# Kernel optimization log

Hardware: AMD Instinct MI355X
Metric: run time of the kernel (lower is better)

The kernel has to match this reference:

```python
import jax, jax.numpy as jnp
import numpy as np

BLOCK = 8  # block_size from init_kwargs


def _zigzag(n):
    # Same traversal as zigzag_indices() in the original module.
    idx = np.zeros(n * n, dtype=np.int64)
    i = j = 0
    for k in range(n * n):
        idx[k] = i * n + j
        if (i + j) % 2 == 0:  # moving up-right
            if j == n - 1:
                i += 1
            elif i == 0:
                j += 1
            else:
                i -= 1
                j += 1
        else:  # moving down-left
            if i == n - 1:
                j += 1
            elif j == 0:
                i += 1
            else:
                i += 1
                j -= 1
    return idx


def _dct_basis(N):
    # dct() with norm=None is DCT-II: V[k] = 2 * sum_n x[n] cos(pi*(2n+1)k/(2N))
    k = np.arange(N)[:, None].astype(np.float64)
    nn = np.arange(N)[None, :].astype(np.float64)
    return (2.0 * np.cos(np.pi * (2.0 * nn + 1.0) * k / (2.0 * N))).astype(np.float32)


def setup_inputs() -> dict:
    key = jax.random.key(0)
    img = jax.random.normal(key, (16, 3, 512, 512), dtype=jnp.float32)
    return {"img": img}


def reference(img):
    B = BLOCK
    bs, c, h, w = img.shape
    hb, wb = h // B, w // B
    n = hb * wb
    m = hb  # square grid: m = sqrt(n)

    # split_blocks: unfold(2,B,B).unfold(3,B,B) -> [bs,c,hb,wb,B,B] -> [bs,n,c,B,B]
    blocks = (
        img.reshape(bs, c, hb, B, wb, B)
        .transpose(0, 2, 4, 1, 3, 5)
        .reshape(bs, n, c, B, B)
    )

    # dct_2d with norm=None as separable matmuls against the DCT-II basis
    C = jnp.asarray(_dct_basis(B))  # [B, B] basis, C[k, x]
    z = jnp.einsum("uh,vw,bnchw->bncuv", C, C, blocks)  # [bs,n,c,B,B]

    # frequencyFeat: zigzag-reorder the B*B coeffs, then tile blocks into an m x m map
    zz = jnp.asarray(_zigzag(B))
    flat = z.reshape(bs, n, c, B * B)[..., zz]  # [bs,n,c,B*B]
    feat = (
        flat.reshape(bs, m, m, c, B * B)
        .transpose(0, 3, 4, 1, 2)
        .reshape(bs, c * B * B, m, m)
    )
    return feat
```

## Files before the change

### kernel.cpp

```cpp
#include <hip/hip_runtime.h>


#define K1 1.9615705608064609f
#define K2 1.8477590650225735f
#define K3 1.6629392246050905f
#define K4 1.4142135623730951f
#define K5 1.1111404660392044f
#define K6 0.7653668647301796f
#define K7 0.3901806440322565f

#define DCT8(x0,x1,x2,x3,x4,x5,x6,x7, y0,y1,y2,y3,y4,y5,y6,y7) do {        \
    float s0=(x0)+(x7), s1=(x1)+(x6), s2=(x2)+(x5), s3=(x3)+(x4);          \
    float d0=(x0)-(x7), d1=(x1)-(x6), d2=(x2)-(x5), d3=(x3)-(x4);          \
    float e0=s0+s3, e1=s1+s2, o0=s0-s3, o1=s1-s2;                          \
    y0 = 2.0f*(e0+e1);                                                     \
    y4 = K4*(e0-e1);                                                       \
    y2 = K2*o0 + K6*o1;                                                    \
    y6 = K6*o0 - K2*o1;                                                    \
    y1 = K1*d0 + K3*d1 + K5*d2 + K7*d3;                                    \
    y3 = K3*d0 - K7*d1 - K1*d2 - K5*d3;                                    \
    y5 = K5*d0 - K1*d1 + K7*d2 + K3*d3;                                    \
    y7 = K7*d0 - K5*d1 + K3*d2 - K1*d3;                                    \
} while (0)

#define LOADROW(r)                                                          \
    const float4 L##r##a = *reinterpret_cast<const float4*>(src + (r)*512); \
    const float4 L##r##b = *reinterpret_cast<const float4*>(src + (r)*512 + 4);

#define ROWDCT(r)                                                          \
    DCT8(L##r##a.x,L##r##a.y,L##r##a.z,L##r##a.w,                          \
         L##r##b.x,L##r##b.y,L##r##b.z,L##r##b.w,                          \
         t##r##0,t##r##1,t##r##2,t##r##3,t##r##4,t##r##5,t##r##6,t##r##7);

#define COLSTORE(v, p0,p1,p2,p3,p4,p5,p6,p7) do {                          \
    float z0,z1,z2,z3,z4,z5,z6,z7;                                         \
    DCT8(t0##v,t1##v,t2##v,t3##v,t4##v,t5##v,t6##v,t7##v,                  \
         z0,z1,z2,z3,z4,z5,z6,z7);                                         \
    __builtin_nontemporal_store(z0, dst + (size_t)(p0)*4096);              \
    __builtin_nontemporal_store(z1, dst + (size_t)(p1)*4096);              \
    __builtin_nontemporal_store(z2, dst + (size_t)(p2)*4096);              \
    __builtin_nontemporal_store(z3, dst + (size_t)(p3)*4096);              \
    __builtin_nontemporal_store(z4, dst + (size_t)(p4)*4096);              \
    __builtin_nontemporal_store(z5, dst + (size_t)(p5)*4096);              \
    __builtin_nontemporal_store(z6, dst + (size_t)(p6)*4096);              \
    __builtin_nontemporal_store(z7, dst + (size_t)(p7)*4096);              \
} while (0)

__global__ __launch_bounds__(256) void dct2d_zigzag_kernel(
    const float* __restrict__ img, float* __restrict__ out)
{
    const int tid = blockIdx.x * 256 + threadIdx.x;
    const int bj = tid & 63;
    const int bi = (tid >> 6) & 63;
    const int bc = tid >> 12;

    const float* __restrict__ src =
        img + (size_t)bc * 262144 + (size_t)bi * 4096 + (size_t)bj * 8;

    float* __restrict__ dst =
        out + (size_t)bc * 262144 + (size_t)bi * 64 + (size_t)bj;

    LOADROW(0) LOADROW(1) LOADROW(2) LOADROW(3)
    LOADROW(4) LOADROW(5) LOADROW(6) LOADROW(7)

    float t00,t01,t02,t03,t04,t05,t06,t07;
    float t10,t11,t12,t13,t14,t15,t16,t17;
    float t20,t21,t22,t23,t24,t25,t26,t27;
    float t30,t31,t32,t33,t34,t35,t36,t37;
    float t40,t41,t42,t43,t44,t45,t46,t47;
    float t50,t51,t52,t53,t54,t55,t56,t57;
    float t60,t61,t62,t63,t64,t65,t66,t67;
    float t70,t71,t72,t73,t74,t75,t76,t77;

    ROWDCT(0) ROWDCT(1) ROWDCT(2) ROWDCT(3)
    ROWDCT(4) ROWDCT(5) ROWDCT(6) ROWDCT(7)

    COLSTORE(0,  0,  2,  3,  9, 10, 20, 21, 35);
    COLSTORE(1,  1,  4,  8, 11, 19, 22, 34, 36);
    COLSTORE(2,  5,  7, 12, 18, 23, 33, 37, 48);
    COLSTORE(3,  6, 13, 17, 24, 32, 38, 47, 49);
    COLSTORE(4, 14, 16, 25, 31, 39, 46, 50, 57);
    COLSTORE(5, 15, 26, 30, 40, 45, 51, 56, 58);
    COLSTORE(6, 27, 29, 41, 44, 52, 55, 59, 62);
    COLSTORE(7, 28, 42, 43, 53, 54, 60, 61, 63);
}

extern "C" void kernel_launch(void* const* d_in, const int* in_sizes, int n_in,
                              void* d_out, int out_size, void* d_ws, size_t ws_size,
                              hipStream_t stream)
{
    const float* img = (const float*)d_in[0];
    float* out = (float*)d_out;
    dct2d_zigzag_kernel<<<768, 256, 0, stream>>>(img, out);
}
```

Measured before the change: 95.39 us.

## Stage zigzag outputs through LDS to emit 16-byte nontemporal vector stores

Each thread still computes one 8x8 block DCT, but the coefficients now go to shared memory in groups of 16 zigzag planes. Each wave then reads back contiguous 256-float rows and writes them to global memory as float4 nontemporal stores. Previously each coefficient was a scalar 4-byte store. Wider stores reduce the number of store instructions and memory transactions. The cost is 16KB of LDS per block and eight barriers, which may reduce occupancy and add synchronisation stalls.

Measured after the change: 96.24 us. Within noise of the previous version (+0.9%).

```diff
diff --git a/kernel.cpp b/kernel.cpp
--- a/kernel.cpp
+++ b/kernel.cpp
@@ -1,5 +1,7 @@
 #include <hip/hip_runtime.h>
 
+
+typedef float floatx4 __attribute__((ext_vector_type(4)));
 
 #define K1 1.9615705608064609f
 #define K2 1.8477590650225735f
@@ -32,33 +34,44 @@
          L##r##b.x,L##r##b.y,L##r##b.z,L##r##b.w,                          \
          t##r##0,t##r##1,t##r##2,t##r##3,t##r##4,t##r##5,t##r##6,t##r##7);
 
-#define COLSTORE(v, p0,p1,p2,p3,p4,p5,p6,p7) do {                          \
-    float z0,z1,z2,z3,z4,z5,z6,z7;                                         \
+#define COLDCT(v)                                                          \
     DCT8(t0##v,t1##v,t2##v,t3##v,t4##v,t5##v,t6##v,t7##v,                  \
-         z0,z1,z2,z3,z4,z5,z6,z7);                                         \
-    __builtin_nontemporal_store(z0, dst + (size_t)(p0)*4096);              \
-    __builtin_nontemporal_store(z1, dst + (size_t)(p1)*4096);              \
-    __builtin_nontemporal_store(z2, dst + (size_t)(p2)*4096);              \
-    __builtin_nontemporal_store(z3, dst + (size_t)(p3)*4096);              \
-    __builtin_nontemporal_store(z4, dst + (size_t)(p4)*4096);              \
-    __builtin_nontemporal_store(z5, dst + (size_t)(p5)*4096);              \
-    __builtin_nontemporal_store(z6, dst + (size_t)(p6)*4096);              \
-    __builtin_nontemporal_store(z7, dst + (size_t)(p7)*4096);              \
+         t0##v,t1##v,t2##v,t3##v,t4##v,t5##v,t6##v,t7##v);
+
+#define LW(u,v,p) lds[((p)&15)*256 + tx] = t##u##v;
+
+#define DRAIN(c) do {                                                      \
+    __syncthreads();                                                       \
+    _Pragma("unroll")                                                      \
+    for (int i = 0; i < 4; ++i) {                                          \
+        const int pl = (tx >> 6) * 4 + i;                \
+        const floatx4 vv =                                                 \
+            *reinterpret_cast<const floatx4*>(&lds[pl*256 + lane*4]);      \
+        __builtin_nontemporal_store(vv,                                    \
+            reinterpret_cast<floatx4*>(dstc + (size_t)((c)*16+pl)*4096     \
+                                       + lane*4));                         \
+    }                                                                      \
+    __syncthreads();                                                       \
 } while (0)
 
 __global__ __launch_bounds__(256) void dct2d_zigzag_kernel(
     const float* __restrict__ img, float* __restrict__ out)
 {
-    const int tid = blockIdx.x * 256 + threadIdx.x;
-    const int bj = tid & 63;
-    const int bi = (tid >> 6) & 63;
-    const int bc = tid >> 12;
+    __shared__ float lds[16 * 256];
+
+    const int tx   = threadIdx.x;
+    const int lane = tx & 63;
+    const int w    = tx >> 6;
+    const int g    = blockIdx.x;
+    const int bc   = g >> 4;
+    const int bi0  = (g & 15) * 4;
+    const int bi   = bi0 + w;
 
     const float* __restrict__ src =
-        img + (size_t)bc * 262144 + (size_t)bi * 4096 + (size_t)bj * 8;
+        img + (size_t)bc * 262144 + (size_t)bi * 4096 + (size_t)lane * 8;
 
-    float* __restrict__ dst =
-        out + (size_t)bc * 262144 + (size_t)bi * 64 + (size_t)bj;
+    float* __restrict__ dstc =
+        out + (size_t)bc * 262144 + (size_t)bi0 * 64;
 
     LOADROW(0) LOADROW(1) LOADROW(2) LOADROW(3)
     LOADROW(4) LOADROW(5) LOADROW(6) LOADROW(7)
@@ -75,14 +88,28 @@
     ROWDCT(0) ROWDCT(1) ROWDCT(2) ROWDCT(3)
     ROWDCT(4) ROWDCT(5) ROWDCT(6) ROWDCT(7)
 
-    COLSTORE(0,  0,  2,  3,  9, 10, 20, 21, 35);
-    COLSTORE(1,  1,  4,  8, 11, 19, 22, 34, 36);
-    COLSTORE(2,  5,  7, 12, 18, 23, 33, 37, 48);
-    COLSTORE(3,  6, 13, 17, 24, 32, 38, 47, 49);
-    COLSTORE(4, 14, 16, 25, 31, 39, 46, 50, 57);
-    COLSTORE(5, 15, 26, 30, 40, 45, 51, 56, 58);
-    COLSTORE(6, 27, 29, 41, 44, 52, 55, 59, 62);
-    COLSTORE(7, 28, 42, 43, 53, 54, 60, 61, 63);
+    COLDCT(0) COLDCT(1) COLDCT(2) COLDCT(3)
+    COLDCT(4) COLDCT(5) COLDCT(6) COLDCT(7)
+
+    LW(0,0, 0) LW(0,1, 1) LW(1,0, 2) LW(2,0, 3) LW(1,1, 4) LW(0,2, 5)
+    LW(0,3, 6) LW(1,2, 7) LW(2,1, 8) LW(3,0, 9) LW(4,0,10) LW(3,1,11)
+    LW(2,2,12) LW(1,3,13) LW(0,4,14) LW(0,5,15)
+    DRAIN(0);
+
+    LW(1,4,16) LW(2,3,17) LW(3,2,18) LW(4,1,19) LW(5,0,20) LW(6,0,21)
+    LW(5,1,22) LW(4,2,23) LW(3,3,24) LW(2,4,25) LW(1,5,26) LW(0,6,27)
+    LW(0,7,28) LW(1,6,29) LW(2,5,30) LW(3,4,31)
+    DRAIN(1);
+
+    LW(4,3,32) LW(5,2,33) LW(6,1,34) LW(7,0,35) LW(7,1,36) LW(6,2,37)
+    LW(5,3,38) LW(4,4,39) LW(3,5,40) LW(2,6,41) LW(1,7,42) LW(2,7,43)
+    LW(3,6,44) LW(4,5,45) LW(5,4,46) LW(6,3,47)
+    DRAIN(2);
+
+    LW(7,2,48) LW(7,3,49) LW(6,4,50) LW(5,5,51) LW(4,6,52) LW(3,7,53)
+    LW(4,7,54) LW(5,6,55) LW(6,5,56) LW(7,4,57) LW(7,5,58) LW(6,6,59)
+    LW(5,7,60) LW(6,7,61) LW(7,6,62) LW(7,7,63)
+    DRAIN(3);
 }
 
 extern "C" void kernel_launch(void* const* d_in, const int* in_sizes, int n_in,
```
